# Performance work log

Measured on AMD Instinct MI355X. Metric: run time of the kernel, lower is better.

## Reference

```python
import jax, jax.numpy as jnp
import numpy as np

HIDDEN = 512
ATT = 512
B, S = 32, 2048


def setup_inputs() -> dict:
    key = jax.random.key(0)
    ks = jax.random.split(key, 9)
    enc_output = jax.random.normal(ks[0], (B, S, 2 * HIDDEN), dtype=jnp.float32)
    decoder_hidden = jax.random.normal(ks[1], (B, HIDDEN), dtype=jnp.float32)
    masks = jax.random.randint(ks[2], (B, S, 1), 0, 2).astype(jnp.bool_)
    # Learned params (init_weights style: uniform(-0.1, 0.1), zero bias)
    W_enc = jax.random.uniform(ks[3], (2 * HIDDEN, ATT), minval=-0.1, maxval=0.1, dtype=jnp.float32)
    b_enc = jnp.zeros((ATT,), dtype=jnp.float32)
    W_dec = jax.random.uniform(ks[4], (HIDDEN, ATT), minval=-0.1, maxval=0.1, dtype=jnp.float32)
    b_dec = jnp.zeros((ATT,), dtype=jnp.float32)
    W_att = jax.random.uniform(ks[5], (ATT, 1), minval=-0.1, maxval=0.1, dtype=jnp.float32)
    b_att = jnp.zeros((1,), dtype=jnp.float32)
    return {
        "enc_output": enc_output,
        "decoder_hidden": decoder_hidden,
        "masks": masks,
        "W_enc": W_enc,
        "b_enc": b_enc,
        "W_dec": W_dec,
        "b_dec": b_dec,
        "W_att": W_att,
        "b_att": b_att,
    }


def reference(enc_output, decoder_hidden, masks, W_enc, b_enc, W_dec, b_dec, W_att, b_att):
    # encoder_att: [B, S, A]
    encoder_att = jnp.einsum("bse,ea->bsa", enc_output, W_enc) + b_enc
    # decoder_att: [B, A]
    decoder_att = decoder_hidden @ W_dec + b_dec
    # scores: [B, S, 1]
    scores = jnp.tanh(encoder_att + decoder_att[:, None, :]) @ W_att + b_att
    scores = jnp.where(masks, -jnp.inf, scores)
    att_weights = jax.nn.softmax(scores, axis=1)  # softmax over seq dim
    # context over encoder_att (note: original weights encoder_att, not enc_output)
    att_context_vector = jnp.sum(encoder_att * att_weights, axis=1)  # [B, A]
    return att_context_vector
```

## Files before the change

kernel.cpp:

```cpp
#include <hip/hip_runtime.h>
#include <math.h>

#define B_  32
#define S_  2048
#define E_  1024
#define A_  512
#define H_  512

#define MB   128
#define NCH  (S_ / MB)
#define KT   32
#define NK   (E_ / KT)

typedef __bf16 bf16;
typedef __attribute__((ext_vector_type(8))) __bf16 bf16x8;
typedef __attribute__((ext_vector_type(4))) float  f32x4;

__device__ __forceinline__ float fast_tanh(float x) {
    x = fminf(fmaxf(x, -15.f), 15.f);
    const float e = __expf(2.f * x);
    return (e - 1.f) / (e + 1.f);
}

__global__ __launch_bounds__(256)
void prep_kernel(const float* __restrict__ Wenc,
                 const float* __restrict__ dh,
                 const float* __restrict__ Wdec,
                 const float* __restrict__ bdec,
                 bf16* __restrict__ Whi, bf16* __restrict__ Wlo,
                 float* __restrict__ dp) {
    const int t = threadIdx.x;
    if (blockIdx.x < 128) {
        __shared__ float tile[64][65];
        const int kb = blockIdx.x >> 3;
        const int ab = blockIdx.x & 7;
        const int k0 = kb * 64, a0 = ab * 64;
#pragma unroll
        for (int p = 0; p < 8; ++p) {
            const int kk = p * 8 + (t >> 5);
            const int aa = (t & 31) * 2;
            const float2 v = *(const float2*)&Wenc[(size_t)(k0 + kk) * A_ + a0 + aa];
            tile[kk][aa]     = v.x;
            tile[kk][aa + 1] = v.y;
        }
        __syncthreads();
        const int aa  = t >> 2;
        const int kk0 = (t & 3) * 16;
        bf16x8 hv0, hv1, lv0, lv1;
#pragma unroll
        for (int j = 0; j < 16; ++j) {
            const float x = tile[kk0 + j][aa];
            const bf16 h = (bf16)x;
            const bf16 l = (bf16)(x - (float)h);
            if (j < 8) { hv0[j] = h; lv0[j] = l; }
            else       { hv1[j - 8] = h; lv1[j - 8] = l; }
        }
        bf16* dh_ = Whi + (size_t)(a0 + aa) * E_ + k0 + kk0;
        bf16* dl_ = Wlo + (size_t)(a0 + aa) * E_ + k0 + kk0;
        *(bf16x8*)dh_ = hv0; *((bf16x8*)dh_ + 1) = hv1;
        *(bf16x8*)dl_ = lv0; *((bf16x8*)dl_ + 1) = lv1;
    } else {
        __shared__ float dhl[64];
        const int idx = blockIdx.x - 128;
        const int b   = idx >> 3;
        const int seg = idx & 7;
        if (t < 64) dhl[t] = dh[b * H_ + seg * 64 + t];
        __syncthreads();
        const int a0 = t, a1 = t + 256;
        float acc0 = 0.f, acc1 = 0.f;
        const float* Wrow = Wdec + (size_t)(seg * 64) * A_;
#pragma unroll 8
        for (int h = 0; h < 64; ++h) {
            const float s = dhl[h];
            acc0 += s * Wrow[h * A_ + a0];
            acc1 += s * Wrow[h * A_ + a1];
        }
        if (seg == 0) { acc0 += bdec[a0]; acc1 += bdec[a1]; }
        dp[(size_t)(seg * B_ + b) * A_ + a0] = acc0;
        dp[(size_t)(seg * B_ + b) * A_ + a1] = acc1;
    }
}

__global__ __launch_bounds__(512, 2)
void fused_kernel(const float* __restrict__ enc,
                  const int*   __restrict__ masks,
                  const bf16*  __restrict__ Whi_g,
                  const bf16*  __restrict__ Wlo_g,
                  const float* __restrict__ benc,
                  const float* __restrict__ Watt,
                  const float* __restrict__ batt,
                  const float* __restrict__ dp,
                  float* __restrict__ pm,
                  float* __restrict__ pl,
                  float* __restrict__ pctx) {
    __shared__ union {
        struct {
            __align__(16) bf16 Ab[2][2][MB * KT];
        } k;
        struct {
            float decl[A_], wattl[A_], bencl[A_];
            float red[MB * 8];
            float score[MB], p[MB];
            int   mask[MB];
        } e;
    } sm;

    const int t    = threadIdx.x;
    const int wv   = t >> 6;
    const int L    = t & 63;
    const int quad = L >> 4;
    const int colL = L & 15;
    const int b    = blockIdx.x >> 4;
    const int ch   = blockIdx.x & 15;
    const int s0   = ch * MB;

    const float* encB = enc + ((size_t)(b * S_ + s0)) * E_;

    f32x4 acc[8][4];
#pragma unroll
    for (int mt = 0; mt < 8; ++mt)
#pragma unroll
        for (int nt = 0; nt < 4; ++nt) acc[mt][nt] = (f32x4){0.f, 0.f, 0.f, 0.f};

    const int arow = t >> 2;
    const int akq  = t & 3;
    const int a_wr = ((arow >> 4) * 512) + akq * 128 +
                     (((arow & 15) ^ (akq << 2)) * 8);
    const float* aptr = encB + (size_t)arow * E_ + akq * 8;
    const int a_rd = quad * 128 + (((L & 15) ^ (quad << 2)) * 8);

    const bf16* wHi = Whi_g + (size_t)(wv * 64 + colL) * E_ + quad * 8;
    const bf16* wLo = Wlo_g + (size_t)(wv * 64 + colL) * E_ + quad * 8;

    bf16x8 bh0[4], bl0[4], bh1[4], bl1[4];
    float4 cA0, cB0, cA1, cB1;

    cA0 = *(const float4*)(aptr);
    cB0 = *(const float4*)(aptr + 4);
#pragma unroll
    for (int nt = 0; nt < 4; ++nt) {
        bh0[nt] = *(const bf16x8*)(wHi + (size_t)nt * (16 * E_));
        bl0[nt] = *(const bf16x8*)(wLo + (size_t)nt * (16 * E_));
    }
    cA1 = *(const float4*)(aptr + KT);
    cB1 = *(const float4*)(aptr + KT + 4);
    {
        const float xs[8] = {cA0.x, cA0.y, cA0.z, cA0.w, cB0.x, cB0.y, cB0.z, cB0.w};
        bf16x8 hv, lv;
#pragma unroll
        for (int j = 0; j < 8; ++j) {
            const bf16 h = (bf16)xs[j];
            hv[j] = h; lv[j] = (bf16)(xs[j] - (float)h);
        }
        *(bf16x8*)&sm.k.Ab[0][0][a_wr] = hv;
        *(bf16x8*)&sm.k.Ab[0][1][a_wr] = lv;
    }
    asm volatile("s_waitcnt lgkmcnt(0)" ::: "memory");
    __builtin_amdgcn_s_barrier();
    asm volatile("" ::: "memory");

#define STEP(KT_, BH, BL, BHN, BLN, PA, PB, QA, QB)                            \
    {                                                                          \
        const int ktn_ = (KT_) + 1;                                            \
        if (ktn_ < NK) {                                                       \
            _Pragma("unroll")                                                  \
            for (int nt = 0; nt < 4; ++nt) {                                   \
                BHN[nt] = *(const bf16x8*)(wHi + (size_t)nt * (16 * E_) +      \
                                           (size_t)ktn_ * KT);                 \
                BLN[nt] = *(const bf16x8*)(wLo + (size_t)nt * (16 * E_) +      \
                                           (size_t)ktn_ * KT);                 \
            }                                                                  \
        }                                                                      \
        if ((KT_) + 2 < NK) {                                                  \
            const float* np_ = aptr + (size_t)((KT_) + 2) * KT;                \
            QA = *(const float4*)(np_);                                        \
            QB = *(const float4*)(np_ + 4);                                    \
        }                                                                      \
        const bf16* Ahi_ = sm.k.Ab[(KT_) & 1][0];                              \
        const bf16* Alo_ = sm.k.Ab[(KT_) & 1][1];                              \
        _Pragma("unroll")                                                      \
        for (int mt = 0; mt < 8; ++mt) {                                       \
            const bf16x8 ah = *(const bf16x8*)&Ahi_[mt * 512 + a_rd];          \
            const bf16x8 al = *(const bf16x8*)&Alo_[mt * 512 + a_rd];          \
            _Pragma("unroll")                                                  \
            for (int nt = 0; nt < 4; ++nt) {                                   \
                acc[mt][nt] = __builtin_amdgcn_mfma_f32_16x16x32_bf16(         \
                    ah, BH[nt], acc[mt][nt], 0, 0, 0);                         \
                acc[mt][nt] = __builtin_amdgcn_mfma_f32_16x16x32_bf16(         \
                    al, BH[nt], acc[mt][nt], 0, 0, 0);                         \
                acc[mt][nt] = __builtin_amdgcn_mfma_f32_16x16x32_bf16(         \
                    ah, BL[nt], acc[mt][nt], 0, 0, 0);                         \
            }                                                                  \
        }                                                                      \
        if (ktn_ < NK) {                                                       \
            const float xs_[8] = {PA.x, PA.y, PA.z, PA.w,                      \
                                  PB.x, PB.y, PB.z, PB.w};                     \
            bf16x8 hv_, lv_;                                                   \
            _Pragma("unroll")                                                  \
            for (int j = 0; j < 8; ++j) {                                      \
                const bf16 h_ = (bf16)xs_[j];                                  \
                hv_[j] = h_; lv_[j] = (bf16)(xs_[j] - (float)h_);              \
            }                                                                  \
            *(bf16x8*)&sm.k.Ab[ktn_ & 1][0][a_wr] = hv_;                       \
            *(bf16x8*)&sm.k.Ab[ktn_ & 1][1][a_wr] = lv_;                       \
            asm volatile("s_waitcnt lgkmcnt(0)" ::: "memory");                 \
            __builtin_amdgcn_s_barrier();                                      \
            asm volatile("" ::: "memory");                                     \
        }                                                                      \
    }

    for (int kt = 0; kt < NK; kt += 2) {
        STEP(kt,     bh0, bl0, bh1, bl1, cA1, cB1, cA0, cB0);
        STEP(kt + 1, bh1, bl1, bh0, bl0, cA0, cB0, cA1, cB1);
    }
#undef STEP

    __syncthreads();
    {
        float d = 0.f;
#pragma unroll
        for (int g = 0; g < 8; ++g) d += dp[(size_t)(g * B_ + b) * A_ + t];
        sm.e.decl[t]  = d;
        sm.e.wattl[t] = Watt[t];
        sm.e.bencl[t] = benc[t];
        if (t < MB) sm.e.mask[t] = masks[(size_t)b * S_ + s0 + t];
    }
    __syncthreads();

    float sp[8][4];
#pragma unroll
    for (int mt = 0; mt < 8; ++mt)
#pragma unroll
        for (int r = 0; r < 4; ++r) sp[mt][r] = 0.f;

#pragma unroll
    for (int nt = 0; nt < 4; ++nt) {
        const int cg = wv * 64 + nt * 16 + colL;
        const float bv  = sm.e.bencl[cg];
        const float dv  = sm.e.decl[cg];
        const float wav = sm.e.wattl[cg];
#pragma unroll
        for (int mt = 0; mt < 8; ++mt)
#pragma unroll
            for (int r = 0; r < 4; ++r) {
                const float ea = acc[mt][nt][r] + bv;
                acc[mt][nt][r] = ea;
                sp[mt][r] += fast_tanh(ea + dv) * wav;
            }
    }
#pragma unroll
    for (int d = 1; d < 16; d <<= 1)
#pragma unroll
        for (int mt = 0; mt < 8; ++mt)
#pragma unroll
            for (int r = 0; r < 4; ++r)
                sp[mt][r] += __shfl_xor(sp[mt][r], d);
    if (colL == 0) {
#pragma unroll
        for (int mt = 0; mt < 8; ++mt)
#pragma unroll
            for (int r = 0; r < 4; ++r)
                sm.e.red[(mt * 16 + quad * 4 + r) * 8 + wv] = sp[mt][r];
    }
    __syncthreads();

    if (t < MB) {
        float s = 0.f;
#pragma unroll
        for (int j = 0; j < 8; ++j) s += sm.e.red[t * 8 + j];
        sm.e.score[t] = s + batt[0];
    }
    __syncthreads();

    float m_loc = -1e30f;
    for (int r = 0; r < MB; ++r)
        if (!sm.e.mask[r]) m_loc = fmaxf(m_loc, sm.e.score[r]);
    if (t < MB) sm.e.p[t] = sm.e.mask[t] ? 0.f : __expf(sm.e.score[t] - m_loc);
    __syncthreads();

    float ctxl[4] = {0.f, 0.f, 0.f, 0.f};
#pragma unroll
    for (int mt = 0; mt < 8; ++mt)
#pragma unroll
        for (int r = 0; r < 4; ++r) {
            const float p = sm.e.p[mt * 16 + quad * 4 + r];
#pragma unroll
            for (int nt = 0; nt < 4; ++nt) ctxl[nt] += p * acc[mt][nt][r];
        }
#pragma unroll
    for (int nt = 0; nt < 4; ++nt) {
        ctxl[nt] += __shfl_xor(ctxl[nt], 16);
        ctxl[nt] += __shfl_xor(ctxl[nt], 32);
    }
    if (quad == 0) {
#pragma unroll
        for (int nt = 0; nt < 4; ++nt)
            pctx[(size_t)blockIdx.x * A_ + wv * 64 + nt * 16 + colL] = ctxl[nt];
    }
    if (t == 0) {
        float l = 0.f;
        for (int r = 0; r < MB; ++r) l += sm.e.p[r];
        pm[blockIdx.x] = m_loc;
        pl[blockIdx.x] = l;
    }
}

__global__ __launch_bounds__(512)
void combine_kernel(const float* __restrict__ pm,
                    const float* __restrict__ pl,
                    const float* __restrict__ pctx,
                    float* __restrict__ out) {
    const int b = blockIdx.x;
    const int t = threadIdx.x;
    float m_g = -1e30f;
    for (int c = 0; c < NCH; ++c) m_g = fmaxf(m_g, pm[b * NCH + c]);
    float L = 0.f;
    for (int c = 0; c < NCH; ++c)
        L += pl[b * NCH + c] * __expf(pm[b * NCH + c] - m_g);
    const float inv = 1.f / L;
    float s = 0.f;
    for (int c = 0; c < NCH; ++c)
        s += pctx[((size_t)b * NCH + c) * A_ + t] * __expf(pm[b * NCH + c] - m_g);
    out[b * A_ + t] = s * inv;
}

extern "C" void kernel_launch(void* const* d_in, const int* in_sizes, int n_in,
                              void* d_out, int out_size, void* d_ws, size_t ws_size,
                              hipStream_t stream) {
    const float* enc  = (const float*)d_in[0];
    const float* dh   = (const float*)d_in[1];
    const int*   mks  = (const int*)  d_in[2];
    const float* Wenc = (const float*)d_in[3];
    const float* benc = (const float*)d_in[4];
    const float* Wdec = (const float*)d_in[5];
    const float* bdec = (const float*)d_in[6];
    const float* Watt = (const float*)d_in[7];
    const float* batt = (const float*)d_in[8];
    float* out = (float*)d_out;

    float* ws   = (float*)d_ws;
    float* pm   = ws;
    float* pl   = pm + B_ * NCH;
    float* pctx = pl + B_ * NCH;
    float* dp   = pctx + (size_t)B_ * NCH * A_;
    bf16*  Whi  = (bf16*)(dp + 8 * B_ * A_);
    bf16*  Wlo  = Whi + (size_t)A_ * E_;
    (void)in_sizes; (void)n_in; (void)out_size; (void)ws_size;

    prep_kernel<<<384, 256, 0, stream>>>(Wenc, dh, Wdec, bdec, Whi, Wlo, dp);
    fused_kernel<<<B_ * NCH, 512, 0, stream>>>(
        enc, mks, Whi, Wlo, benc, Watt, batt, dp, pm, pl, pctx);
    combine_kernel<<<B_, 512, 0, stream>>>(pm, pl, pctx, out);
}
```

Before: 534.1 us.

## Double fused kernel block to 1024 threads, halving per-wave output columns

The fused GEMM+attention kernel now runs 16 waves per block instead of 8. Each wave owns 32 attention columns instead of 64, which halves the accumulator registers and the B-fragment loads per wave. Each thread stages 4 floats of the encoder tile instead of 8. The score reduction buffer is widened to 16 partials per row with a padded stride of 17. The aim is more resident waves to hide memory and MFMA latency, at the cost of more barrier participants and a larger cross-wave reduction; the 1024,4 launch bound may push register limits.

```diff
diff --git a/kernel.cpp b/kernel.cpp
--- a/kernel.cpp
+++ b/kernel.cpp
@@ -14,6 +14,7 @@
 
 typedef __bf16 bf16;
 typedef __attribute__((ext_vector_type(8))) __bf16 bf16x8;
+typedef __attribute__((ext_vector_type(4))) __bf16 bf16x4;
 typedef __attribute__((ext_vector_type(4))) float  f32x4;
 
 __device__ __forceinline__ float fast_tanh(float x) {
@@ -81,7 +82,7 @@
     }
 }
 
-__global__ __launch_bounds__(512, 2)
+__global__ __launch_bounds__(1024, 4)
 void fused_kernel(const float* __restrict__ enc,
                   const int*   __restrict__ masks,
                   const bf16*  __restrict__ Whi_g,
@@ -99,7 +100,7 @@
         } k;
         struct {
             float decl[A_], wattl[A_], bencl[A_];
-            float red[MB * 8];
+            float red[MB * 17];
             float score[MB], p[MB];
             int   mask[MB];
         } e;
@@ -116,55 +117,55 @@
 
     const float* encB = enc + ((size_t)(b * S_ + s0)) * E_;
 
-    f32x4 acc[8][4];
+    f32x4 acc[8][2];
 #pragma unroll
     for (int mt = 0; mt < 8; ++mt)
 #pragma unroll
-        for (int nt = 0; nt < 4; ++nt) acc[mt][nt] = (f32x4){0.f, 0.f, 0.f, 0.f};
-
-    const int arow = t >> 2;
-    const int akq  = t & 3;
+        for (int nt = 0; nt < 2; ++nt) acc[mt][nt] = (f32x4){0.f, 0.f, 0.f, 0.f};
+
+    const int arow = t >> 3;
+    const int akq  = (t & 7) >> 1;
+    const int ahh  = t & 1;
     const int a_wr = ((arow >> 4) * 512) + akq * 128 +
-                     (((arow & 15) ^ (akq << 2)) * 8);
-    const float* aptr = encB + (size_t)arow * E_ + akq * 8;
+                     (((arow & 15) ^ (akq << 2)) * 8) + ahh * 4;
+    const float* aptr = encB + (size_t)arow * E_ + (t & 7) * 4;
     const int a_rd = quad * 128 + (((L & 15) ^ (quad << 2)) * 8);
 
-    const bf16* wHi = Whi_g + (size_t)(wv * 64 + colL) * E_ + quad * 8;
-    const bf16* wLo = Wlo_g + (size_t)(wv * 64 + colL) * E_ + quad * 8;
-
-    bf16x8 bh0[4], bl0[4], bh1[4], bl1[4];
-    float4 cA0, cB0, cA1, cB1;
+    const size_t woff = (size_t)(wv * 32 + colL) * E_ + quad * 8;
+    const bf16* wHi = Whi_g + woff;
+    const bf16* wLo = Wlo_g + woff;
+
+    bf16x8 bh0[2], bl0[2], bh1[2], bl1[2];
+    float4 cA0, cA1;
 
     cA0 = *(const float4*)(aptr);
-    cB0 = *(const float4*)(aptr + 4);
-#pragma unroll
-    for (int nt = 0; nt < 4; ++nt) {
+#pragma unroll
+    for (int nt = 0; nt < 2; ++nt) {
         bh0[nt] = *(const bf16x8*)(wHi + (size_t)nt * (16 * E_));
         bl0[nt] = *(const bf16x8*)(wLo + (size_t)nt * (16 * E_));
     }
     cA1 = *(const float4*)(aptr + KT);
-    cB1 = *(const float4*)(aptr + KT + 4);
     {
-        const float xs[8] = {cA0.x, cA0.y, cA0.z, cA0.w, cB0.x, cB0.y, cB0.z, cB0.w};
-        bf16x8 hv, lv;
-#pragma unroll
-        for (int j = 0; j < 8; ++j) {
+        const float xs[4] = {cA0.x, cA0.y, cA0.z, cA0.w};
+        bf16x4 hv, lv;
+#pragma unroll
+        for (int j = 0; j < 4; ++j) {
             const bf16 h = (bf16)xs[j];
             hv[j] = h; lv[j] = (bf16)(xs[j] - (float)h);
         }
-        *(bf16x8*)&sm.k.Ab[0][0][a_wr] = hv;
-        *(bf16x8*)&sm.k.Ab[0][1][a_wr] = lv;
+        *(bf16x4*)&sm.k.Ab[0][0][a_wr] = hv;
+        *(bf16x4*)&sm.k.Ab[0][1][a_wr] = lv;
     }
     asm volatile("s_waitcnt lgkmcnt(0)" ::: "memory");
     __builtin_amdgcn_s_barrier();
     asm volatile("" ::: "memory");
 
-#define STEP(KT_, BH, BL, BHN, BLN, PA, PB, QA, QB)                            \
+#define STEP(KT_, BH, BL, BHN, BLN, PA, QA)                                    \
     {                                                                          \
         const int ktn_ = (KT_) + 1;                                            \
         if (ktn_ < NK) {                                                       \
             _Pragma("unroll")                                                  \
-            for (int nt = 0; nt < 4; ++nt) {                                   \
+            for (int nt = 0; nt < 2; ++nt) {                                   \
                 BHN[nt] = *(const bf16x8*)(wHi + (size_t)nt * (16 * E_) +      \
                                            (size_t)ktn_ * KT);                 \
                 BLN[nt] = *(const bf16x8*)(wLo + (size_t)nt * (16 * E_) +      \
@@ -172,9 +173,7 @@
             }                                                                  \
         }                                                                      \
         if ((KT_) + 2 < NK) {                                                  \
-            const float* np_ = aptr + (size_t)((KT_) + 2) * KT;                \
-            QA = *(const float4*)(np_);                                        \
-            QB = *(const float4*)(np_ + 4);                                    \
+            QA = *(const float4*)(aptr + (size_t)((KT_) + 2) * KT);            \
         }                                                                      \
         const bf16* Ahi_ = sm.k.Ab[(KT_) & 1][0];                              \
         const bf16* Alo_ = sm.k.Ab[(KT_) & 1][1];                              \
@@ -183,7 +182,7 @@
             const bf16x8 ah = *(const bf16x8*)&Ahi_[mt * 512 + a_rd];          \
             const bf16x8 al = *(const bf16x8*)&Alo_[mt * 512 + a_rd];          \
             _Pragma("unroll")                                                  \
-            for (int nt = 0; nt < 4; ++nt) {                                   \
+            for (int nt = 0; nt < 2; ++nt) {                                   \
                 acc[mt][nt] = __builtin_amdgcn_mfma_f32_16x16x32_bf16(         \
                     ah, BH[nt], acc[mt][nt], 0, 0, 0);                         \
                 acc[mt][nt] = __builtin_amdgcn_mfma_f32_16x16x32_bf16(         \
@@ -193,16 +192,15 @@
             }                                                                  \
         }                                                                      \
         if (ktn_ < NK) {                                                       \
-            const float xs_[8] = {PA.x, PA.y, PA.z, PA.w,                      \
-                                  PB.x, PB.y, PB.z, PB.w};                     \
-            bf16x8 hv_, lv_;                                                   \
+            const float xs_[4] = {PA.x, PA.y, PA.z, PA.w};                     \
+            bf16x4 hv_, lv_;                                                   \
             _Pragma("unroll")                                                  \
-            for (int j = 0; j < 8; ++j) {                                      \
+            for (int j = 0; j < 4; ++j) {                                      \
                 const bf16 h_ = (bf16)xs_[j];                                  \
                 hv_[j] = h_; lv_[j] = (bf16)(xs_[j] - (float)h_);              \
             }                                                                  \
-            *(bf16x8*)&sm.k.Ab[ktn_ & 1][0][a_wr] = hv_;                       \
-            *(bf16x8*)&sm.k.Ab[ktn_ & 1][1][a_wr] = lv_;                       \
+            *(bf16x4*)&sm.k.Ab[ktn_ & 1][0][a_wr] = hv_;                       \
+            *(bf16x4*)&sm.k.Ab[ktn_ & 1][1][a_wr] = lv_;                       \
             asm volatile("s_waitcnt lgkmcnt(0)" ::: "memory");                 \
             __builtin_amdgcn_s_barrier();                                      \
             asm volatile("" ::: "memory");                                     \
@@ -210,13 +208,13 @@
     }
 
     for (int kt = 0; kt < NK; kt += 2) {
-        STEP(kt,     bh0, bl0, bh1, bl1, cA1, cB1, cA0, cB0);
-        STEP(kt + 1, bh1, bl1, bh0, bl0, cA0, cB0, cA1, cB1);
+        STEP(kt,     bh0, bl0, bh1, bl1, cA1, cA0);
+        STEP(kt + 1, bh1, bl1, bh0, bl0, cA0, cA1);
     }
 #undef STEP
 
     __syncthreads();
-    {
+    if (t < A_) {
         float d = 0.f;
 #pragma unroll
         for (int g = 0; g < 8; ++g) d += dp[(size_t)(g * B_ + b) * A_ + t];
@@ -234,8 +232,8 @@
         for (int r = 0; r < 4; ++r) sp[mt][r] = 0.f;
 
 #pragma unroll
-    for (int nt = 0; nt < 4; ++nt) {
-        const int cg = wv * 64 + nt * 16 + colL;
+    for (int nt = 0; nt < 2; ++nt) {
+        const int cg = wv * 32 + nt * 16 + colL;
         const float bv  = sm.e.bencl[cg];
         const float dv  = sm.e.decl[cg];
         const float wav = sm.e.wattl[cg];
@@ -260,14 +258,14 @@
         for (int mt = 0; mt < 8; ++mt)
 #pragma unroll
             for (int r = 0; r < 4; ++r)
-                sm.e.red[(mt * 16 + quad * 4 + r) * 8 + wv] = sp[mt][r];
+                sm.e.red[(mt * 16 + quad * 4 + r) * 17 + wv] = sp[mt][r];
     }
     __syncthreads();
 
     if (t < MB) {
         float s = 0.f;
 #pragma unroll
-        for (int j = 0; j < 8; ++j) s += sm.e.red[t * 8 + j];
+        for (int j = 0; j < 16; ++j) s += sm.e.red[t * 17 + j];
         sm.e.score[t] = s + batt[0];
     }
     __syncthreads();
@@ -278,24 +276,24 @@
     if (t < MB) sm.e.p[t] = sm.e.mask[t] ? 0.f : __expf(sm.e.score[t] - m_loc);
     __syncthreads();
 
-    float ctxl[4] = {0.f, 0.f, 0.f, 0.f};
+    float ctxl[2] = {0.f, 0.f};
 #pragma unroll
     for (int mt = 0; mt < 8; ++mt)
 #pragma unroll
         for (int r = 0; r < 4; ++r) {
             const float p = sm.e.p[mt * 16 + quad * 4 + r];
 #pragma unroll
-            for (int nt = 0; nt < 4; ++nt) ctxl[nt] += p * acc[mt][nt][r];
-        }
-#pragma unroll
-    for (int nt = 0; nt < 4; ++nt) {
+            for (int nt = 0; nt < 2; ++nt) ctxl[nt] += p * acc[mt][nt][r];
+        }
+#pragma unroll
+    for (int nt = 0; nt < 2; ++nt) {
         ctxl[nt] += __shfl_xor(ctxl[nt], 16);
         ctxl[nt] += __shfl_xor(ctxl[nt], 32);
     }
     if (quad == 0) {
 #pragma unroll
-        for (int nt = 0; nt < 4; ++nt)
-            pctx[(size_t)blockIdx.x * A_ + wv * 64 + nt * 16 + colL] = ctxl[nt];
+        for (int nt = 0; nt < 2; ++nt)
+            pctx[(size_t)blockIdx.x * A_ + wv * 32 + nt * 16 + colL] = ctxl[nt];
     }
     if (t == 0) {
         float l = 0.f;
@@ -348,7 +346,7 @@
     (void)in_sizes; (void)n_in; (void)out_size; (void)ws_size;
 
     prep_kernel<<<384, 256, 0, stream>>>(Wenc, dh, Wdec, bdec, Whi, Wlo, dp);
-    fused_kernel<<<B_ * NCH, 512, 0, stream>>>(
+    fused_kernel<<<B_ * NCH, 1024, 0, stream>>>(
         enc, mks, Whi, Wlo, benc, Watt, batt, dp, pm, pl, pctx);
     combine_kernel<<<B_, 512, 0, stream>>>(pm, pl, pctx, out);
 }
```

New measurement: 546.8 us. 1.02x slower.

## Halve row tile to 64, widen K stage to 64, raise occupancy to 4 blocks

Applied to the files above, without the earlier changes.

Each block now covers 64 sequence rows instead of 128, doubling the grid to 32 chunks per batch and shrinking the accumulator array. The launch bound moves from 2 to 4 blocks per CU. The K loop now stages 64 columns per barrier, split into two 32-wide sub-blocks, and loads W fragments directly per sub-block without the register double buffer. The aim is to hide latency through occupancy and fewer barriers, at the cost of re-reading W from global for twice as many blocks, producing twice as many partial results to combine, and losing the explicit prefetch of the B operand.

```diff
diff --git a/kernel.cpp b/kernel.cpp
--- a/kernel.cpp
+++ b/kernel.cpp
@@ -7,10 +7,11 @@
 #define A_  512
 #define H_  512
 
-#define MB   128
+#define MB   64
 #define NCH  (S_ / MB)
 #define KT   32
-#define NK   (E_ / KT)
+#define BK   64
+#define NP   (E_ / BK)
 
 typedef __bf16 bf16;
 typedef __attribute__((ext_vector_type(8))) __bf16 bf16x8;
@@ -81,7 +82,7 @@
     }
 }
 
-__global__ __launch_bounds__(512, 2)
+__global__ __launch_bounds__(512, 4)
 void fused_kernel(const float* __restrict__ enc,
                   const int*   __restrict__ masks,
                   const bf16*  __restrict__ Whi_g,
@@ -95,11 +96,11 @@
                   float* __restrict__ pctx) {
     __shared__ union {
         struct {
-            __align__(16) bf16 Ab[2][2][MB * KT];
+            __align__(16) bf16 Ab[2][2][2][2048];
         } k;
         struct {
             float decl[A_], wattl[A_], bencl[A_];
-            float red[MB * 8];
+            float red[MB * 9];
             float score[MB], p[MB];
             int   mask[MB];
         } e;
@@ -110,110 +111,101 @@
     const int L    = t & 63;
     const int quad = L >> 4;
     const int colL = L & 15;
-    const int b    = blockIdx.x >> 4;
-    const int ch   = blockIdx.x & 15;
+    const int b    = blockIdx.x >> 5;
+    const int ch   = blockIdx.x & 31;
     const int s0   = ch * MB;
 
     const float* encB = enc + ((size_t)(b * S_ + s0)) * E_;
 
-    f32x4 acc[8][4];
-#pragma unroll
-    for (int mt = 0; mt < 8; ++mt)
+    f32x4 acc[4][4];
+#pragma unroll
+    for (int mt = 0; mt < 4; ++mt)
 #pragma unroll
         for (int nt = 0; nt < 4; ++nt) acc[mt][nt] = (f32x4){0.f, 0.f, 0.f, 0.f};
 
-    const int arow = t >> 2;
-    const int akq  = t & 3;
-    const int a_wr = ((arow >> 4) * 512) + akq * 128 +
+    const int arow = t >> 3;
+    const int k0   = (t & 7) * 8;
+    const int asub = k0 >> 5;
+    const int akq  = (k0 & 31) >> 3;
+    const int a_wr = (arow >> 4) * 512 + akq * 128 +
                      (((arow & 15) ^ (akq << 2)) * 8);
-    const float* aptr = encB + (size_t)arow * E_ + akq * 8;
-    const int a_rd = quad * 128 + (((L & 15) ^ (quad << 2)) * 8);
-
-    const bf16* wHi = Whi_g + (size_t)(wv * 64 + colL) * E_ + quad * 8;
-    const bf16* wLo = Wlo_g + (size_t)(wv * 64 + colL) * E_ + quad * 8;
-
-    bf16x8 bh0[4], bl0[4], bh1[4], bl1[4];
-    float4 cA0, cB0, cA1, cB1;
-
-    cA0 = *(const float4*)(aptr);
-    cB0 = *(const float4*)(aptr + 4);
-#pragma unroll
-    for (int nt = 0; nt < 4; ++nt) {
-        bh0[nt] = *(const bf16x8*)(wHi + (size_t)nt * (16 * E_));
-        bl0[nt] = *(const bf16x8*)(wLo + (size_t)nt * (16 * E_));
-    }
-    cA1 = *(const float4*)(aptr + KT);
-    cB1 = *(const float4*)(aptr + KT + 4);
+    const float* aptr = encB + (size_t)arow * E_ + k0;
+    const int a_rd = quad * 128 + ((colL ^ (quad << 2)) * 8);
+
+    const size_t woff = (size_t)(wv * 64 + colL) * E_ + quad * 8;
+    const bf16* wHi = Whi_g + woff;
+    const bf16* wLo = Wlo_g + woff;
+
     {
-        const float xs[8] = {cA0.x, cA0.y, cA0.z, cA0.w, cB0.x, cB0.y, cB0.z, cB0.w};
+        const float4 c0 = *(const float4*)(aptr);
+        const float4 c1 = *(const float4*)(aptr + 4);
+        const float xs[8] = {c0.x, c0.y, c0.z, c0.w, c1.x, c1.y, c1.z, c1.w};
         bf16x8 hv, lv;
 #pragma unroll
         for (int j = 0; j < 8; ++j) {
             const bf16 h = (bf16)xs[j];
             hv[j] = h; lv[j] = (bf16)(xs[j] - (float)h);
         }
-        *(bf16x8*)&sm.k.Ab[0][0][a_wr] = hv;
-        *(bf16x8*)&sm.k.Ab[0][1][a_wr] = lv;
+        *(bf16x8*)&sm.k.Ab[0][asub][0][a_wr] = hv;
+        *(bf16x8*)&sm.k.Ab[0][asub][1][a_wr] = lv;
     }
     asm volatile("s_waitcnt lgkmcnt(0)" ::: "memory");
     __builtin_amdgcn_s_barrier();
     asm volatile("" ::: "memory");
 
-#define STEP(KT_, BH, BL, BHN, BLN, PA, PB, QA, QB)                            \
+#define KKBLOCK(KG_, SUB_)                                                     \
     {                                                                          \
-        const int ktn_ = (KT_) + 1;                                            \
-        if (ktn_ < NK) {                                                       \
-            _Pragma("unroll")                                                  \
-            for (int nt = 0; nt < 4; ++nt) {                                   \
-                BHN[nt] = *(const bf16x8*)(wHi + (size_t)nt * (16 * E_) +      \
-                                           (size_t)ktn_ * KT);                 \
-                BLN[nt] = *(const bf16x8*)(wLo + (size_t)nt * (16 * E_) +      \
-                                           (size_t)ktn_ * KT);                 \
-            }                                                                  \
+        bf16x8 bh[4], bl[4];                                                   \
+        _Pragma("unroll")                                                      \
+        for (int nt = 0; nt < 4; ++nt) {                                       \
+            bh[nt] = *(const bf16x8*)(wHi + (size_t)nt * (16 * E_) + (KG_));   \
+            bl[nt] = *(const bf16x8*)(wLo + (size_t)nt * (16 * E_) + (KG_));   \
         }                                                                      \
-        if ((KT_) + 2 < NK) {                                                  \
-            const float* np_ = aptr + (size_t)((KT_) + 2) * KT;                \
-            QA = *(const float4*)(np_);                                        \
-            QB = *(const float4*)(np_ + 4);                                    \
-        }                                                                      \
-        const bf16* Ahi_ = sm.k.Ab[(KT_) & 1][0];                              \
-        const bf16* Alo_ = sm.k.Ab[(KT_) & 1][1];                              \
+        const bf16* Ahi_ = &sm.k.Ab[buf][SUB_][0][0];                          \
+        const bf16* Alo_ = &sm.k.Ab[buf][SUB_][1][0];                          \
         _Pragma("unroll")                                                      \
-        for (int mt = 0; mt < 8; ++mt) {                                       \
+        for (int mt = 0; mt < 4; ++mt) {                                       \
             const bf16x8 ah = *(const bf16x8*)&Ahi_[mt * 512 + a_rd];          \
             const bf16x8 al = *(const bf16x8*)&Alo_[mt * 512 + a_rd];          \
             _Pragma("unroll")                                                  \
             for (int nt = 0; nt < 4; ++nt) {                                   \
                 acc[mt][nt] = __builtin_amdgcn_mfma_f32_16x16x32_bf16(         \
-                    ah, BH[nt], acc[mt][nt], 0, 0, 0);                         \
+                    ah, bh[nt], acc[mt][nt], 0, 0, 0);                         \
                 acc[mt][nt] = __builtin_amdgcn_mfma_f32_16x16x32_bf16(         \
-                    al, BH[nt], acc[mt][nt], 0, 0, 0);                         \
+                    al, bh[nt], acc[mt][nt], 0, 0, 0);                         \
                 acc[mt][nt] = __builtin_amdgcn_mfma_f32_16x16x32_bf16(         \
-                    ah, BL[nt], acc[mt][nt], 0, 0, 0);                         \
+                    ah, bl[nt], acc[mt][nt], 0, 0, 0);                         \
             }                                                                  \
         }                                                                      \
-        if (ktn_ < NK) {                                                       \
-            const float xs_[8] = {PA.x, PA.y, PA.z, PA.w,                      \
-                                  PB.x, PB.y, PB.z, PB.w};                     \
-            bf16x8 hv_, lv_;                                                   \
-            _Pragma("unroll")                                                  \
-            for (int j = 0; j < 8; ++j) {                                      \
-                const bf16 h_ = (bf16)xs_[j];                                  \
-                hv_[j] = h_; lv_[j] = (bf16)(xs_[j] - (float)h_);              \
-            }                                                                  \
-            *(bf16x8*)&sm.k.Ab[ktn_ & 1][0][a_wr] = hv_;                       \
-            *(bf16x8*)&sm.k.Ab[ktn_ & 1][1][a_wr] = lv_;                       \
-            asm volatile("s_waitcnt lgkmcnt(0)" ::: "memory");                 \
-            __builtin_amdgcn_s_barrier();                                      \
-            asm volatile("" ::: "memory");                                     \
-        }                                                                      \
-    }
-
-    for (int kt = 0; kt < NK; kt += 2) {
-        STEP(kt,     bh0, bl0, bh1, bl1, cA1, cB1, cA0, cB0);
-        STEP(kt + 1, bh1, bl1, bh0, bl0, cA0, cB0, cA1, cB1);
-    }
-#undef STEP
+    }
+
+    for (int p = 0; p < NP; ++p) {
+        const int buf = p & 1;
+        const bool more = (p + 1 < NP);
+        float4 c0, c1;
+        if (more) {
+            const float* np = aptr + (size_t)(p + 1) * BK;
+            c0 = *(const float4*)(np);
+            c1 = *(const float4*)(np + 4);
+        }
+        KKBLOCK(p * BK, 0);
+        if (more) {
+            const float xs[8] = {c0.x, c0.y, c0.z, c0.w, c1.x, c1.y, c1.z, c1.w};
+            bf16x8 hv, lv;
+#pragma unroll
+            for (int j = 0; j < 8; ++j) {
+                const bf16 h = (bf16)xs[j];
+                hv[j] = h; lv[j] = (bf16)(xs[j] - (float)h);
+            }
+            *(bf16x8*)&sm.k.Ab[buf ^ 1][asub][0][a_wr] = hv;
+            *(bf16x8*)&sm.k.Ab[buf ^ 1][asub][1][a_wr] = lv;
+        }
+        KKBLOCK(p * BK + KT, 1);
+        asm volatile("s_waitcnt lgkmcnt(0)" ::: "memory");
+        __builtin_amdgcn_s_barrier();
+        asm volatile("" ::: "memory");
+    }
+#undef KKBLOCK
 
     __syncthreads();
     {
@@ -227,9 +219,9 @@
     }
     __syncthreads();
 
-    float sp[8][4];
-#pragma unroll
-    for (int mt = 0; mt < 8; ++mt)
+    float sp[4][4];
+#pragma unroll
+    for (int mt = 0; mt < 4; ++mt)
 #pragma unroll
         for (int r = 0; r < 4; ++r) sp[mt][r] = 0.f;
 
@@ -240,7 +232,7 @@
         const float dv  = sm.e.decl[cg];
         const float wav = sm.e.wattl[cg];
 #pragma unroll
-        for (int mt = 0; mt < 8; ++mt)
+        for (int mt = 0; mt < 4; ++mt)
 #pragma unroll
             for (int r = 0; r < 4; ++r) {
                 const float ea = acc[mt][nt][r] + bv;
@@ -251,23 +243,23 @@
 #pragma unroll
     for (int d = 1; d < 16; d <<= 1)
 #pragma unroll
-        for (int mt = 0; mt < 8; ++mt)
+        for (int mt = 0; mt < 4; ++mt)
 #pragma unroll
             for (int r = 0; r < 4; ++r)
                 sp[mt][r] += __shfl_xor(sp[mt][r], d);
     if (colL == 0) {
 #pragma unroll
-        for (int mt = 0; mt < 8; ++mt)
+        for (int mt = 0; mt < 4; ++mt)
 #pragma unroll
             for (int r = 0; r < 4; ++r)
-                sm.e.red[(mt * 16 + quad * 4 + r) * 8 + wv] = sp[mt][r];
+                sm.e.red[(mt * 16 + quad * 4 + r) * 9 + wv] = sp[mt][r];
     }
     __syncthreads();
 
     if (t < MB) {
         float s = 0.f;
 #pragma unroll
-        for (int j = 0; j < 8; ++j) s += sm.e.red[t * 8 + j];
+        for (int j = 0; j < 8; ++j) s += sm.e.red[t * 9 + j];
         sm.e.score[t] = s + batt[0];
     }
     __syncthreads();
@@ -280,7 +272,7 @@
 
     float ctxl[4] = {0.f, 0.f, 0.f, 0.f};
 #pragma unroll
-    for (int mt = 0; mt < 8; ++mt)
+    for (int mt = 0; mt < 4; ++mt)
 #pragma unroll
         for (int r = 0; r < 4; ++r) {
             const float p = sm.e.p[mt * 16 + quad * 4 + r];
```

Result: slower. 662.5 us (+24.0%).
